# Optimization experiments

Measured on AMD Instinct MI355X. Metric: run time of the kernel, lower is better.

## Reference

```python
import jax, jax.numpy as jnp
import numpy as np

B, S, HID = 2, 2048, 2048
NH, NKV = 16, 4
HD = HID // NH            # 128
N_REP = NH // NKV          # 4
THETA = 10000.0
NEG = -1e9


def _rope_tables(position_ids):
    # inv_freq: [HD/2]
    inv_freq = 1.0 / (THETA ** (jnp.arange(0, HD, 2, dtype=jnp.float32) / HD))
    freqs = position_ids.astype(jnp.float32)[..., None] * inv_freq  # [B,S,HD/2]
    emb = jnp.concatenate([freqs, freqs], axis=-1)                  # [B,S,HD]
    return jnp.cos(emb), jnp.sin(emb)


def _rotate_half(x):
    return jnp.concatenate([-x[..., HD // 2:], x[..., :HD // 2]], axis=-1)


def setup_inputs() -> dict:
    key = jax.random.key(0)
    k1, k2, k3 = jax.random.split(key, 3)
    hidden_states = jax.random.normal(k1, (B, S, HID), dtype=jnp.float32)
    w_qkv = jax.random.normal(k2, (HID + 2 * NKV * HD, HID), dtype=jnp.float32) * 0.02
    w_out = jax.random.normal(k3, (HID, HID), dtype=jnp.float32) * 0.02
    causal = jnp.tril(jnp.ones((S, S), dtype=bool))
    attention_mask = jnp.where(causal, 0.0, NEG).astype(jnp.float32)
    attention_mask = jnp.broadcast_to(attention_mask[None, None], (B, 1, S, S))
    position_ids = jnp.broadcast_to(jnp.arange(S, dtype=jnp.int64), (B, S))
    return {"hidden_states": hidden_states, "w_qkv": w_qkv, "w_out": w_out,
            "attention_mask": attention_mask, "position_ids": position_ids}


def reference(hidden_states, w_qkv, w_out, attention_mask, position_ids):
    bsz, q_len, _ = hidden_states.shape
    qkv = hidden_states @ w_qkv.T                                   # [B,S,HID+2*NKV*HD]
    q, k, v = jnp.split(qkv, [HID, HID + NKV * HD], axis=-1)
    q = q.reshape(bsz, q_len, NH, HD).transpose(0, 2, 1, 3)         # [B,NH,S,HD]
    k = k.reshape(bsz, q_len, NKV, HD).transpose(0, 2, 1, 3)        # [B,NKV,S,HD]
    v = v.reshape(bsz, q_len, NKV, HD).transpose(0, 2, 1, 3)

    cos, sin = _rope_tables(position_ids)                           # [B,S,HD]
    cos, sin = cos[:, None], sin[:, None]                           # unsqueeze head dim
    q = q * cos + _rotate_half(q) * sin
    k = k * cos + _rotate_half(k) * sin

    # GQA: repeat KV heads to match query heads (repeat_kv)
    k = jnp.repeat(k, N_REP, axis=1)                                # [B,NH,S,HD]
    v = jnp.repeat(v, N_REP, axis=1)

    scale = 1.0 / jnp.sqrt(jnp.float32(HD))
    scores = jnp.einsum('bhqd,bhkd->bhqk', q, k) * scale
    scores = scores + attention_mask                                # [B,NH,S,S]
    attn = jax.nn.softmax(scores.astype(jnp.float32), axis=-1).astype(q.dtype)
    out = jnp.einsum('bhqk,bhkd->bhqd', attn, v)                    # [B,NH,S,HD]
    out = out.transpose(0, 2, 1, 3).reshape(bsz, q_len, HID)
    return out @ w_out.T
```

## Files before the change

kernel.cpp:

```cpp
#include <hip/hip_runtime.h>
#include <hip/hip_bf16.h>
#include <math.h>

#define S_LEN   2048
#define HIDDEN  2048
#define NHEADS  16
#define NKVH    4
#define HDIM    128

typedef short  short8  __attribute__((ext_vector_type(8)));
typedef float  floatx4 __attribute__((ext_vector_type(4)));
typedef __hip_bfloat16 bf16;

__device__ inline void async_copy16(const void* g, void* l) {
  __builtin_amdgcn_global_load_lds((__attribute__((address_space(1))) void*)(g),
                                   (__attribute__((address_space(3))) void*)(l),
                                   16, 0, 0);
}

__device__ inline unsigned short cvt1(float x) {
  bf16 t = __float2bfloat16(x);
  return *reinterpret_cast<unsigned short*>(&t);
}
__device__ inline float us2f(unsigned short u) {
  unsigned int v = ((unsigned int)u) << 16;
  return *reinterpret_cast<float*>(&v);
}

#define N8_H  1048576
#define N8_WQ  786432
#define N8_WO  524288
__global__ __launch_bounds__(256) void cvt_all(const float* __restrict__ h,
                                               const float* __restrict__ wq,
                                               const float* __restrict__ wo,
                                               unsigned short* __restrict__ dst) {
  const int i = blockIdx.x * 256 + threadIdx.x;
  if (i >= N8_H + N8_WQ + N8_WO) return;
  const float* src; int j;
  if (i < N8_H)              { src = h;  j = i; }
  else if (i < N8_H + N8_WQ) { src = wq; j = i - N8_H; }
  else                       { src = wo; j = i - N8_H - N8_WQ; }
  const float4 a = reinterpret_cast<const float4*>(src)[j * 2];
  const float4 b = reinterpret_cast<const float4*>(src)[j * 2 + 1];
  unsigned short o[8] = {cvt1(a.x), cvt1(a.y), cvt1(a.z), cvt1(a.w),
                         cvt1(b.x), cvt1(b.y), cvt1(b.z), cvt1(b.w)};
  *reinterpret_cast<short8*>(dst + (size_t)i * 8) = *reinterpret_cast<short8*>(o);
}

template<int MODE>
__global__ __launch_bounds__(256) void gemm_bt(const bf16* __restrict__ A,
                                               const bf16* __restrict__ B,
                                               int M, int N, int K,
                                               bf16* __restrict__ qbuf,
                                               bf16* __restrict__ kbuf,
                                               bf16* __restrict__ vtbuf,
                                               float* __restrict__ Cout)
{
  __shared__ unsigned short As[128 * 32];
  __shared__ unsigned short Bs[128 * 32];
  const int t    = threadIdx.x;
  const int w    = t >> 6;
  const int lane = t & 63;
  const int m16  = lane & 15;
  const int quad = lane >> 4;
  const int wm   = (w >> 1) * 64;
  const int wn   = (w & 1) * 64;
  const int bm   = blockIdx.y, bn = blockIdx.x;

  const floatx4 zf = {0.f, 0.f, 0.f, 0.f};
  floatx4 acc[4][4];
#pragma unroll
  for (int i = 0; i < 4; ++i)
#pragma unroll
    for (int j = 0; j < 4; ++j) acc[i][j] = zf;

  const bf16* gA = A + (size_t)(bm * 128 + (t >> 2)) * K + (t & 3) * 8;
  const bf16* gB = B + (size_t)(bn * 128 + (t >> 2)) * K + (t & 3) * 8;
  unsigned short* lA = &As[w * 512];
  unsigned short* lB = &Bs[w * 512];

  for (int k0 = 0; k0 < K; k0 += 32) {
    __syncthreads();
#pragma unroll
    for (int i = 0; i < 2; ++i) {
      async_copy16(gA + (size_t)(64 * i) * K + k0, lA + i * 2048);
      async_copy16(gB + (size_t)(64 * i) * K + k0, lB + i * 2048);
    }
    __builtin_amdgcn_s_waitcnt(0);
    __syncthreads();
    short8 af[4], bfr[4];
#pragma unroll
    for (int mi = 0; mi < 4; ++mi)
      af[mi] = *reinterpret_cast<const short8*>(&As[(wm + mi * 16 + m16) * 32 + quad * 8]);
#pragma unroll
    for (int ni = 0; ni < 4; ++ni)
      bfr[ni] = *reinterpret_cast<const short8*>(&Bs[(wn + ni * 16 + m16) * 32 + quad * 8]);
#pragma unroll
    for (int mi = 0; mi < 4; ++mi)
#pragma unroll
      for (int ni = 0; ni < 4; ++ni)
        acc[mi][ni] = __builtin_amdgcn_mfma_f32_16x16x32_bf16(af[mi], bfr[ni], acc[mi][ni], 0, 0, 0);
  }

#pragma unroll
  for (int mi = 0; mi < 4; ++mi)
#pragma unroll
    for (int ni = 0; ni < 4; ++ni) {
      const int row0 = bm * 128 + wm + mi * 16 + quad * 4;
      const int col  = bn * 128 + wn + ni * 16 + m16;
#pragma unroll
      for (int r = 0; r < 4; ++r) {
        const float v = acc[mi][ni][r];
        const int m = row0 + r;
        if (MODE == 0) {
          const int b = m >> 11, s = m & 2047;
          if (col < HIDDEN) {
            const int hh = col >> 7, d = col & 127;
            qbuf[(((size_t)(b * NHEADS + hh)) * S_LEN + s) * HDIM + d] = __float2bfloat16(v);
          } else if (col < HIDDEN + NKVH * HDIM) {
            const int nn = col - HIDDEN; const int hh = nn >> 7, d = nn & 127;
            kbuf[(((size_t)(b * NKVH + hh)) * S_LEN + s) * HDIM + d] = __float2bfloat16(v);
          } else {
            const int nn = col - HIDDEN - NKVH * HDIM; const int hh = nn >> 7, d = nn & 127;
            vtbuf[(((size_t)(b * NKVH + hh)) * HDIM + d) * S_LEN + s] = __float2bfloat16(v);
          }
        } else {
          Cout[(size_t)m * N + col] = v;
        }
      }
    }
}

__global__ __launch_bounds__(256) void rope_kernel(bf16* __restrict__ qbuf,
                                                   bf16* __restrict__ kbuf)
{
  const int idx = blockIdx.x * 256 + threadIdx.x;
  const int QC = 2 * NHEADS * S_LEN * 64;
  bf16* base; int s, j; float post;
  if (idx < QC) {
    j = idx & 63; const int tt = idx >> 6; s = tt & (S_LEN - 1);
    base = qbuf + (size_t)tt * HDIM;
    post = 0.08838834764831845f;
  } else {
    const int k = idx - QC;
    j = k & 63; const int tt = k >> 6; s = tt & (S_LEN - 1);
    base = kbuf + (size_t)tt * HDIM;
    post = 1.0f;
  }
  const float inv = exp2f((float)j * -0.2076205059f);
  const float ang = (float)s * inv;
  float sn, c;
  __sincosf(ang, &sn, &c);
  const float x0 = __bfloat162float(base[j]);
  const float x1 = __bfloat162float(base[j + 64]);
  base[j]      = __float2bfloat16((x0 * c - x1 * sn) * post);
  base[j + 64] = __float2bfloat16((x1 * c + x0 * sn) * post);
}

__global__ __launch_bounds__(256) void attn_partial(const bf16* __restrict__ qbuf,
                                                    const bf16* __restrict__ kbuf,
                                                    const bf16* __restrict__ vtbuf,
                                                    unsigned short* __restrict__ pnum,
                                                    float* __restrict__ plsum)
{
  __shared__ unsigned short Ks[2][4096];
  __shared__ unsigned short Vs[2][4096];
  __shared__ unsigned short Ps[4][640];
  const int i = blockIdx.x >> 1, c = blockIdx.x & 1;
  const int len = (i >> 1) + 1;
  const int nch = (len + 31) >> 5;
  if (c >= nch) return;
  const int half = (len + 1) >> 1;
  const int k0 = (nch == 1) ? 0   : (c ? half : 0);
  const int k1 = (nch == 1) ? len : (c ? len  : half);
  const int kvh = blockIdx.y, b = blockIdx.z;
  const int t = threadIdx.x, w = t >> 6, lane = t & 63;
  const int m16 = lane & 15, quad = lane >> 4;
  const int h = kvh * 4 + w;

  const bf16* Qp = qbuf + (((size_t)(b * NHEADS + h)) * S_LEN + i * 16 + m16) * HDIM;
  short8 qf[4];
#pragma unroll
  for (int cc = 0; cc < 4; ++cc)
    qf[cc] = *reinterpret_cast<const short8*>(Qp + cc * 32 + quad * 8);

  const bf16* Kp  = kbuf  + ((size_t)(b * NKVH + kvh)) * S_LEN * HDIM;
  const bf16* Vtp = vtbuf + ((size_t)(b * NKVH + kvh)) * HDIM * S_LEN;

  const int kk = lane >> 4, cK = lane & 15;
  const int rKa = w * 8 + kk, rKb = rKa + 4;
  const int offKa = rKa * 128 + ((cK ^ (rKa & 7)) * 8);
  const int offKb = rKb * 128 + ((cK ^ (rKb & 7)) * 8);
  const int dd = lane >> 2, cV = lane & 3;
  const int dVa = w * 32 + dd, dVb = dVa + 16;
  const int offVa = dVa * 2048 + ((cV ^ ((dVa >> 1) & 3)) * 8);
  const int offVb = dVb * 2048 + ((cV ^ ((dVb >> 1) & 3)) * 8);

  const floatx4 zf = {0.f, 0.f, 0.f, 0.f};
  floatx4 oacc[8];
#pragma unroll
  for (int d = 0; d < 8; ++d) oacc[d] = zf;
  floatx4 lacc = zf;
  unsigned short ones_s[8] = {0x3F80,0x3F80,0x3F80,0x3F80,0x3F80,0x3F80,0x3F80,0x3F80};
  const short8 ones = *reinterpret_cast<short8*>(ones_s);

  unsigned short* Pw = &Ps[w][0];
  const int myrow = i * 16 + quad * 4;

  {
    const int ks = k0 * 32;
    async_copy16(Kp + (size_t)ks * 128 + offKa, &Ks[0][w * 1024]);
    async_copy16(Kp + (size_t)ks * 128 + offKb, &Ks[0][w * 1024 + 512]);
    async_copy16(Vtp + ks + offVa, &Vs[0][w * 1024]);
    async_copy16(Vtp + ks + offVb, &Vs[0][w * 1024 + 512]);
  }
  __syncthreads();

  for (int ki = k0; ki < k1; ++ki) {
    const int buf = (ki - k0) & 1;
    if (ki + 1 < k1) {
      const int ks = (ki + 1) * 32;
      async_copy16(Kp + (size_t)ks * 128 + offKa, &Ks[buf ^ 1][w * 1024]);
      async_copy16(Kp + (size_t)ks * 128 + offKb, &Ks[buf ^ 1][w * 1024 + 512]);
      async_copy16(Vtp + ks + offVa, &Vs[buf ^ 1][w * 1024]);
      async_copy16(Vtp + ks + offVb, &Vs[buf ^ 1][w * 1024 + 512]);
    }
    const int ks = ki * 32;
    floatx4 s0 = zf, s1 = zf;
#pragma unroll
    for (int cc = 0; cc < 4; ++cc) {
      const int sw = ((cc * 4 + quad) ^ (m16 & 7)) * 8;
      short8 kf0 = *reinterpret_cast<const short8*>(&Ks[buf][m16 * 128 + sw]);
      short8 kf1 = *reinterpret_cast<const short8*>(&Ks[buf][(16 + m16) * 128 + sw]);
      s0 = __builtin_amdgcn_mfma_f32_16x16x32_bf16(qf[cc], kf0, s0, 0, 0, 0);
      s1 = __builtin_amdgcn_mfma_f32_16x16x32_bf16(qf[cc], kf1, s1, 0, 0, 0);
    }
#pragma unroll
    for (int r = 0; r < 4; ++r) {
      const int row = myrow + r;
      const float p0 = (ks + m16      > row) ? 0.f : __expf(s0[r]);
      const float p1 = (ks + 16 + m16 > row) ? 0.f : __expf(s1[r]);
      Pw[(quad * 4 + r) * 40 + m16]      = cvt1(p0);
      Pw[(quad * 4 + r) * 40 + 16 + m16] = cvt1(p1);
    }
    const short8 pa = *reinterpret_cast<const short8*>(&Pw[m16 * 40 + quad * 8]);
    lacc = __builtin_amdgcn_mfma_f32_16x16x32_bf16(pa, ones, lacc, 0, 0, 0);
#pragma unroll
    for (int dt = 0; dt < 8; ++dt) {
      short8 vfr = *reinterpret_cast<const short8*>(
          &Vs[buf][(dt * 16 + m16) * 32 + ((quad ^ ((m16 >> 1) & 3)) * 8)]);
      oacc[dt] = __builtin_amdgcn_mfma_f32_16x16x32_bf16(pa, vfr, oacc[dt], 0, 0, 0);
    }
    __syncthreads();
  }

  const int a = i >> 1, g = a >> 5;
  const int base = 2 * (a + (a & 31) * g) + (i & 1) * (g + 1);
  const int slot = (b * NHEADS + h) * 192 + base + c;
  unsigned short* np = pnum + (size_t)slot * 2048;
#pragma unroll
  for (int dt = 0; dt < 8; ++dt)
#pragma unroll
    for (int r = 0; r < 4; ++r)
      np[(quad * 4 + r) * 128 + dt * 16 + m16] = cvt1(oacc[dt][r]);
  if (m16 == 0) {
#pragma unroll
    for (int r = 0; r < 4; ++r)
      plsum[slot * 16 + quad * 4 + r] = lacc[r];
  }
}

__global__ __launch_bounds__(256) void attn_combine(const unsigned short* __restrict__ pnum,
                                                    const float* __restrict__ plsum,
                                                    bf16* __restrict__ abuf)
{
  const int i = blockIdx.x, h = blockIdx.y, b = blockIdx.z;
  const int t = threadIdx.x, row = t >> 4, c0 = (t & 15) * 8;
  const int a = i >> 1, g = a >> 5;
  const int base = 2 * (a + (a & 31) * g) + (i & 1) * (g + 1);
  const int nch = g + 1;
  const int hb = (b * NHEADS + h) * 192 + base;
  float acc[8] = {0.f,0.f,0.f,0.f,0.f,0.f,0.f,0.f};
  float lsum = 0.f;
  for (int c = 0; c < nch; ++c) {
    const unsigned short* np = pnum + (size_t)(hb + c) * 2048 + row * 128 + c0;
    const short8 v = *reinterpret_cast<const short8*>(np);
#pragma unroll
    for (int j = 0; j < 8; ++j) acc[j] += us2f(((unsigned short*)&v)[j]);
    lsum += plsum[(hb + c) * 16 + row];
  }
  const float invl = 1.0f / lsum;
  unsigned short o[8];
#pragma unroll
  for (int j = 0; j < 8; ++j) o[j] = cvt1(acc[j] * invl);
  *reinterpret_cast<short8*>(abuf + (((size_t)b * S_LEN + i * 16 + row) * NHEADS + h) * HDIM + c0)
      = *reinterpret_cast<short8*>(o);
}

extern "C" void kernel_launch(void* const* d_in, const int* in_sizes, int n_in,
                              void* d_out, int out_size, void* d_ws, size_t ws_size,
                              hipStream_t stream) {
  const float* hidden_f = (const float*)d_in[0];
  const float* wqkv_f   = (const float*)d_in[1];
  const float* wout_f   = (const float*)d_in[2];
  float* out = (float*)d_out;

  char* ws = (char*)d_ws;
  bf16* hbf    = (bf16*)(ws);
  bf16* wqkvbf = (bf16*)(ws + 16777216);
  bf16* woutbf = (bf16*)(ws + 29360128);
  bf16* qbuf   = (bf16*)(ws + 37748736);
  bf16* kbuf   = (bf16*)(ws + 54525952);
  bf16* vtbuf  = (bf16*)(ws + 58720256);
  bf16* abuf   = (bf16*)(ws + 62914560);
  unsigned short* pnum = (unsigned short*)(ws);
  float* plsum = (float*)(ws + 79691776);

  cvt_all<<<9216, 256, 0, stream>>>(hidden_f, wqkv_f, wout_f, (unsigned short*)ws);

  gemm_bt<0><<<dim3(24, 32), 256, 0, stream>>>(hbf, wqkvbf, 4096, 3072, 2048,
                                               qbuf, kbuf, vtbuf, nullptr);
  rope_kernel<<<20480, 256, 0, stream>>>(qbuf, kbuf);
  attn_partial<<<dim3(256, 4, 2), 256, 0, stream>>>(qbuf, kbuf, vtbuf, pnum, plsum);
  attn_combine<<<dim3(128, 16, 2), 256, 0, stream>>>(pnum, plsum, abuf);
  gemm_bt<1><<<dim3(16, 32), 256, 0, stream>>>(abuf, woutbf, 4096, 2048, 2048,
                                               nullptr, nullptr, nullptr, out);
}
```

Measured before the change: 362.8 us.

## Fuse RoPE into QKV GEMM epilogue and process 32 query rows per attention block

Removes the separate RoPE kernel by applying the rotation (and the Q scaling) in the QKV GEMM epilogue. Partner-half values are exchanged between paired warps through shared memory. The attention partial kernel now handles two 16-row query tiles per block, reusing each loaded K/V tile for twice the rows and halving the grid. This changes the partial-sum slot layout and the combine indexing. It saves a full read-modify-write pass over Q/K and some K/V reload traffic, at the cost of more registers, extra epilogue barriers, and fewer blocks for parallelism.

After: 387.2 us. 6.7% more time.

```diff
diff --git a/kernel.cpp b/kernel.cpp
--- a/kernel.cpp
+++ b/kernel.cpp
@@ -56,8 +56,9 @@
                                                bf16* __restrict__ vtbuf,
                                                float* __restrict__ Cout)
 {
-  __shared__ unsigned short As[128 * 32];
-  __shared__ unsigned short Bs[128 * 32];
+  __shared__ unsigned short smem[8192];
+  unsigned short* As = smem;
+  unsigned short* Bs = smem + 4096;
   const int t    = threadIdx.x;
   const int w    = t >> 6;
   const int lane = t & 63;
@@ -102,59 +103,82 @@
         acc[mi][ni] = __builtin_amdgcn_mfma_f32_16x16x32_bf16(af[mi], bfr[ni], acc[mi][ni], 0, 0, 0);
   }
 
-#pragma unroll
-  for (int mi = 0; mi < 4; ++mi)
-#pragma unroll
-    for (int ni = 0; ni < 4; ++ni) {
+  if (MODE == 1) {
+#pragma unroll
+    for (int mi = 0; mi < 4; ++mi)
+#pragma unroll
+      for (int ni = 0; ni < 4; ++ni) {
+        const int row0 = bm * 128 + wm + mi * 16 + quad * 4;
+        const int col  = bn * 128 + wn + ni * 16 + m16;
+#pragma unroll
+        for (int r = 0; r < 4; ++r)
+          Cout[(size_t)(row0 + r) * N + col] = acc[mi][ni][r];
+      }
+    return;
+  }
+
+  const int colbase = bn * 128;
+  if (colbase < HIDDEN + NKVH * HDIM) {
+    const bool isQ = (colbase < HIDDEN);
+    const float post = isQ ? 0.08838834764831845f : 1.0f;
+    float invf[4];
+#pragma unroll
+    for (int ni = 0; ni < 4; ++ni)
+      invf[ni] = exp2f((float)(ni * 16 + m16) * -0.2076205059f);
+    float* L = (float*)smem;
+    __syncthreads();
+#pragma unroll
+    for (int mi = 0; mi < 4; ++mi) {
+#pragma unroll
+      for (int ni = 0; ni < 4; ++ni)
+#pragma unroll
+        for (int r = 0; r < 4; ++r)
+          L[w * 1024 + lane * 16 + ni * 4 + r] = acc[mi][ni][r];
+      __syncthreads();
       const int row0 = bm * 128 + wm + mi * 16 + quad * 4;
-      const int col  = bn * 128 + wn + ni * 16 + m16;
-#pragma unroll
-      for (int r = 0; r < 4; ++r) {
-        const float v = acc[mi][ni][r];
-        const int m = row0 + r;
-        if (MODE == 0) {
-          const int b = m >> 11, s = m & 2047;
-          if (col < HIDDEN) {
+#pragma unroll
+      for (int ni = 0; ni < 4; ++ni) {
+        const int col = colbase + wn + ni * 16 + m16;
+#pragma unroll
+        for (int r = 0; r < 4; ++r) {
+          const float v  = acc[mi][ni][r];
+          const float v2 = L[(w ^ 1) * 1024 + lane * 16 + ni * 4 + r];
+          const int m = row0 + r;
+          const int s = m & 2047;
+          const float ang = (float)s * invf[ni];
+          float sn, cs;
+          __sincosf(ang, &sn, &cs);
+          const float rot = ((w & 1) ? (v * cs + v2 * sn) : (v * cs - v2 * sn)) * post;
+          const int b = m >> 11;
+          if (isQ) {
             const int hh = col >> 7, d = col & 127;
-            qbuf[(((size_t)(b * NHEADS + hh)) * S_LEN + s) * HDIM + d] = __float2bfloat16(v);
-          } else if (col < HIDDEN + NKVH * HDIM) {
+            qbuf[(((size_t)(b * NHEADS + hh)) * S_LEN + s) * HDIM + d] = __float2bfloat16(rot);
+          } else {
             const int nn = col - HIDDEN; const int hh = nn >> 7, d = nn & 127;
-            kbuf[(((size_t)(b * NKVH + hh)) * S_LEN + s) * HDIM + d] = __float2bfloat16(v);
-          } else {
-            const int nn = col - HIDDEN - NKVH * HDIM; const int hh = nn >> 7, d = nn & 127;
-            vtbuf[(((size_t)(b * NKVH + hh)) * HDIM + d) * S_LEN + s] = __float2bfloat16(v);
+            kbuf[(((size_t)(b * NKVH + hh)) * S_LEN + s) * HDIM + d] = __float2bfloat16(rot);
           }
-        } else {
-          Cout[(size_t)m * N + col] = v;
         }
       }
-    }
-}
-
-__global__ __launch_bounds__(256) void rope_kernel(bf16* __restrict__ qbuf,
-                                                   bf16* __restrict__ kbuf)
-{
-  const int idx = blockIdx.x * 256 + threadIdx.x;
-  const int QC = 2 * NHEADS * S_LEN * 64;
-  bf16* base; int s, j; float post;
-  if (idx < QC) {
-    j = idx & 63; const int tt = idx >> 6; s = tt & (S_LEN - 1);
-    base = qbuf + (size_t)tt * HDIM;
-    post = 0.08838834764831845f;
+      __syncthreads();
+    }
   } else {
-    const int k = idx - QC;
-    j = k & 63; const int tt = k >> 6; s = tt & (S_LEN - 1);
-    base = kbuf + (size_t)tt * HDIM;
-    post = 1.0f;
-  }
-  const float inv = exp2f((float)j * -0.2076205059f);
-  const float ang = (float)s * inv;
-  float sn, c;
-  __sincosf(ang, &sn, &c);
-  const float x0 = __bfloat162float(base[j]);
-  const float x1 = __bfloat162float(base[j + 64]);
-  base[j]      = __float2bfloat16((x0 * c - x1 * sn) * post);
-  base[j + 64] = __float2bfloat16((x1 * c + x0 * sn) * post);
+#pragma unroll
+    for (int mi = 0; mi < 4; ++mi)
+#pragma unroll
+      for (int ni = 0; ni < 4; ++ni) {
+        const int row0 = bm * 128 + wm + mi * 16 + quad * 4;
+        const int col  = colbase + wn + ni * 16 + m16;
+        const int nn = col - HIDDEN - NKVH * HDIM;
+        const int hh = nn >> 7, d = nn & 127;
+#pragma unroll
+        for (int r = 0; r < 4; ++r) {
+          const int m = row0 + r;
+          const int b = m >> 11, s = m & 2047;
+          vtbuf[(((size_t)(b * NKVH + hh)) * HDIM + d) * S_LEN + s] =
+              __float2bfloat16(acc[mi][ni][r]);
+        }
+      }
+  }
 }
 
 __global__ __launch_bounds__(256) void attn_partial(const bf16* __restrict__ qbuf,
@@ -165,9 +189,9 @@
 {
   __shared__ unsigned short Ks[2][4096];
   __shared__ unsigned short Vs[2][4096];
-  __shared__ unsigned short Ps[4][640];
-  const int i = blockIdx.x >> 1, c = blockIdx.x & 1;
-  const int len = (i >> 1) + 1;
+  __shared__ unsigned short Ps[4][1280];
+  const int i2 = blockIdx.x >> 1, c = blockIdx.x & 1;
+  const int len = i2 + 1;
   const int nch = (len + 31) >> 5;
   if (c >= nch) return;
   const int half = (len + 1) >> 1;
@@ -178,11 +202,13 @@
   const int m16 = lane & 15, quad = lane >> 4;
   const int h = kvh * 4 + w;
 
-  const bf16* Qp = qbuf + (((size_t)(b * NHEADS + h)) * S_LEN + i * 16 + m16) * HDIM;
-  short8 qf[4];
-#pragma unroll
-  for (int cc = 0; cc < 4; ++cc)
-    qf[cc] = *reinterpret_cast<const short8*>(Qp + cc * 32 + quad * 8);
+  const bf16* Qp = qbuf + (((size_t)(b * NHEADS + h)) * S_LEN + i2 * 32 + m16) * HDIM;
+  short8 qf[2][4];
+#pragma unroll
+  for (int T = 0; T < 2; ++T)
+#pragma unroll
+    for (int cc = 0; cc < 4; ++cc)
+      qf[T][cc] = *reinterpret_cast<const short8*>(Qp + (size_t)T * 16 * HDIM + cc * 32 + quad * 8);
 
   const bf16* Kp  = kbuf  + ((size_t)(b * NKVH + kvh)) * S_LEN * HDIM;
   const bf16* Vtp = vtbuf + ((size_t)(b * NKVH + kvh)) * HDIM * S_LEN;
@@ -197,15 +223,16 @@
   const int offVb = dVb * 2048 + ((cV ^ ((dVb >> 1) & 3)) * 8);
 
   const floatx4 zf = {0.f, 0.f, 0.f, 0.f};
-  floatx4 oacc[8];
-#pragma unroll
-  for (int d = 0; d < 8; ++d) oacc[d] = zf;
-  floatx4 lacc = zf;
+  floatx4 oacc[2][8];
+#pragma unroll
+  for (int T = 0; T < 2; ++T)
+#pragma unroll
+    for (int d = 0; d < 8; ++d) oacc[T][d] = zf;
+  floatx4 lacc[2] = {zf, zf};
   unsigned short ones_s[8] = {0x3F80,0x3F80,0x3F80,0x3F80,0x3F80,0x3F80,0x3F80,0x3F80};
   const short8 ones = *reinterpret_cast<short8*>(ones_s);
 
   unsigned short* Pw = &Ps[w][0];
-  const int myrow = i * 16 + quad * 4;
 
   {
     const int ks = k0 * 32;
@@ -226,47 +253,60 @@
       async_copy16(Vtp + ks + offVb, &Vs[buf ^ 1][w * 1024 + 512]);
     }
     const int ks = ki * 32;
-    floatx4 s0 = zf, s1 = zf;
+    floatx4 s00 = zf, s01 = zf, s10 = zf, s11 = zf;
 #pragma unroll
     for (int cc = 0; cc < 4; ++cc) {
       const int sw = ((cc * 4 + quad) ^ (m16 & 7)) * 8;
       short8 kf0 = *reinterpret_cast<const short8*>(&Ks[buf][m16 * 128 + sw]);
       short8 kf1 = *reinterpret_cast<const short8*>(&Ks[buf][(16 + m16) * 128 + sw]);
-      s0 = __builtin_amdgcn_mfma_f32_16x16x32_bf16(qf[cc], kf0, s0, 0, 0, 0);
-      s1 = __builtin_amdgcn_mfma_f32_16x16x32_bf16(qf[cc], kf1, s1, 0, 0, 0);
-    }
-#pragma unroll
-    for (int r = 0; r < 4; ++r) {
-      const int row = myrow + r;
-      const float p0 = (ks + m16      > row) ? 0.f : __expf(s0[r]);
-      const float p1 = (ks + 16 + m16 > row) ? 0.f : __expf(s1[r]);
-      Pw[(quad * 4 + r) * 40 + m16]      = cvt1(p0);
-      Pw[(quad * 4 + r) * 40 + 16 + m16] = cvt1(p1);
-    }
-    const short8 pa = *reinterpret_cast<const short8*>(&Pw[m16 * 40 + quad * 8]);
-    lacc = __builtin_amdgcn_mfma_f32_16x16x32_bf16(pa, ones, lacc, 0, 0, 0);
+      s00 = __builtin_amdgcn_mfma_f32_16x16x32_bf16(qf[0][cc], kf0, s00, 0, 0, 0);
+      s01 = __builtin_amdgcn_mfma_f32_16x16x32_bf16(qf[0][cc], kf1, s01, 0, 0, 0);
+      s10 = __builtin_amdgcn_mfma_f32_16x16x32_bf16(qf[1][cc], kf0, s10, 0, 0, 0);
+      s11 = __builtin_amdgcn_mfma_f32_16x16x32_bf16(qf[1][cc], kf1, s11, 0, 0, 0);
+    }
+#pragma unroll
+    for (int T = 0; T < 2; ++T) {
+      const floatx4& sa = T ? s10 : s00;
+      const floatx4& sb = T ? s11 : s01;
+#pragma unroll
+      for (int r = 0; r < 4; ++r) {
+        const int row = i2 * 32 + T * 16 + quad * 4 + r;
+        const float p0 = (ks + m16      > row) ? 0.f : __expf(sa[r]);
+        const float p1 = (ks + 16 + m16 > row) ? 0.f : __expf(sb[r]);
+        Pw[(T * 16 + quad * 4 + r) * 40 + m16]      = cvt1(p0);
+        Pw[(T * 16 + quad * 4 + r) * 40 + 16 + m16] = cvt1(p1);
+      }
+    }
+    const short8 pa0 = *reinterpret_cast<const short8*>(&Pw[m16 * 40 + quad * 8]);
+    const short8 pa1 = *reinterpret_cast<const short8*>(&Pw[(16 + m16) * 40 + quad * 8]);
+    lacc[0] = __builtin_amdgcn_mfma_f32_16x16x32_bf16(pa0, ones, lacc[0], 0, 0, 0);
+    lacc[1] = __builtin_amdgcn_mfma_f32_16x16x32_bf16(pa1, ones, lacc[1], 0, 0, 0);
 #pragma unroll
     for (int dt = 0; dt < 8; ++dt) {
       short8 vfr = *reinterpret_cast<const short8*>(
           &Vs[buf][(dt * 16 + m16) * 32 + ((quad ^ ((m16 >> 1) & 3)) * 8)]);
-      oacc[dt] = __builtin_amdgcn_mfma_f32_16x16x32_bf16(pa, vfr, oacc[dt], 0, 0, 0);
+      oacc[0][dt] = __builtin_amdgcn_mfma_f32_16x16x32_bf16(pa0, vfr, oacc[0][dt], 0, 0, 0);
+      oacc[1][dt] = __builtin_amdgcn_mfma_f32_16x16x32_bf16(pa1, vfr, oacc[1][dt], 0, 0, 0);
     }
     __syncthreads();
   }
 
-  const int a = i >> 1, g = a >> 5;
-  const int base = 2 * (a + (a & 31) * g) + (i & 1) * (g + 1);
-  const int slot = (b * NHEADS + h) * 192 + base + c;
-  unsigned short* np = pnum + (size_t)slot * 2048;
-#pragma unroll
-  for (int dt = 0; dt < 8; ++dt)
-#pragma unroll
-    for (int r = 0; r < 4; ++r)
-      np[(quad * 4 + r) * 128 + dt * 16 + m16] = cvt1(oacc[dt][r]);
+  const int base = (i2 < 32) ? i2 : (2 * i2 - 32);
+  const int slot = (b * NHEADS + h) * 96 + base + c;
+  unsigned short* np = pnum + (size_t)slot * 4096;
+#pragma unroll
+  for (int T = 0; T < 2; ++T)
+#pragma unroll
+    for (int dt = 0; dt < 8; ++dt)
+#pragma unroll
+      for (int r = 0; r < 4; ++r)
+        np[(T * 16 + quad * 4 + r) * 128 + dt * 16 + m16] = cvt1(oacc[T][dt][r]);
   if (m16 == 0) {
 #pragma unroll
-    for (int r = 0; r < 4; ++r)
-      plsum[slot * 16 + quad * 4 + r] = lacc[r];
+    for (int T = 0; T < 2; ++T)
+#pragma unroll
+      for (int r = 0; r < 4; ++r)
+        plsum[slot * 32 + T * 16 + quad * 4 + r] = lacc[T][r];
   }
 }
 
@@ -275,25 +315,26 @@
                                                     bf16* __restrict__ abuf)
 {
   const int i = blockIdx.x, h = blockIdx.y, b = blockIdx.z;
-  const int t = threadIdx.x, row = t >> 4, c0 = (t & 15) * 8;
-  const int a = i >> 1, g = a >> 5;
-  const int base = 2 * (a + (a & 31) * g) + (i & 1) * (g + 1);
-  const int nch = g + 1;
-  const int hb = (b * NHEADS + h) * 192 + base;
+  const int i2 = i >> 1, lr0 = (i & 1) * 16;
+  const int t = threadIdx.x, row16 = t >> 4, c0 = (t & 15) * 8;
+  const int lr = lr0 + row16;
+  const int len = i2 + 1, nch = (len + 31) >> 5;
+  const int base = (i2 < 32) ? i2 : (2 * i2 - 32);
+  const int hb = (b * NHEADS + h) * 96 + base;
   float acc[8] = {0.f,0.f,0.f,0.f,0.f,0.f,0.f,0.f};
   float lsum = 0.f;
   for (int c = 0; c < nch; ++c) {
-    const unsigned short* np = pnum + (size_t)(hb + c) * 2048 + row * 128 + c0;
+    const unsigned short* np = pnum + (size_t)(hb + c) * 4096 + lr * 128 + c0;
     const short8 v = *reinterpret_cast<const short8*>(np);
 #pragma unroll
     for (int j = 0; j < 8; ++j) acc[j] += us2f(((unsigned short*)&v)[j]);
-    lsum += plsum[(hb + c) * 16 + row];
+    lsum += plsum[(hb + c) * 32 + lr];
   }
   const float invl = 1.0f / lsum;
   unsigned short o[8];
 #pragma unroll
   for (int j = 0; j < 8; ++j) o[j] = cvt1(acc[j] * invl);
-  *reinterpret_cast<short8*>(abuf + (((size_t)b * S_LEN + i * 16 + row) * NHEADS + h) * HDIM + c0)
+  *reinterpret_cast<short8*>(abuf + (((size_t)b * S_LEN + i * 16 + row16) * NHEADS + h) * HDIM + c0)
       = *reinterpret_cast<short8*>(o);
 }
 
@@ -320,8 +361,7 @@
 
   gemm_bt<0><<<dim3(24, 32), 256, 0, stream>>>(hbf, wqkvbf, 4096, 3072, 2048,
                                                qbuf, kbuf, vtbuf, nullptr);
-  rope_kernel<<<20480, 256, 0, stream>>>(qbuf, kbuf);
-  attn_partial<<<dim3(256, 4, 2), 256, 0, stream>>>(qbuf, kbuf, vtbuf, pnum, plsum);
+  attn_partial<<<dim3(128, 4, 2), 256, 0, stream>>>(qbuf, kbuf, vtbuf, pnum, plsum);
   attn_combine<<<dim3(128, 16, 2), 256, 0, stream>>>(pnum, plsum, abuf);
   gemm_bt<1><<<dim3(16, 32), 256, 0, stream>>>(abuf, woutbf, 4096, 2048, 2048,
                                                nullptr, nullptr, nullptr, out);
```
